# Kernel optimization log

Measured on AMD Instinct MI355X. Metric: run time of the kernel, lower is better.

The kernel has to match this reference:

```python
import jax, jax.numpy as jnp
import numpy as np

HEADS = 8
DIM_HEAD = 32  # dim // heads


def setup_inputs() -> dict:
    key = jax.random.key(0)
    ks = jax.random.split(key, 5)
    B, C, H, W = 4, 256, 48, 48
    return {
        "x": jax.random.normal(ks[0], (B, C, H, W), jnp.float32),
        "Wqkv": jax.random.normal(ks[1], (3 * C, C), jnp.float32) * (C ** -0.5),
        "bqkv": jax.random.normal(ks[2], (3 * C,), jnp.float32) * 0.02,
        "W0": jax.random.normal(ks[3], (C, C), jnp.float32) * (C ** -0.5),
        "b0": jax.random.normal(ks[4], (C,), jnp.float32) * 0.02,
    }


def reference(x, Wqkv, bqkv, W0, b0):
    b, c, h, w = x.shape
    m, d = HEADS, DIM_HEAD
    n = h * w
    scale = d ** -0.5
    # 1x1 conv == per-pixel GEMM: [b,3c,h,w]
    qkv = jnp.einsum('bchw,oc->bohw', x, Wqkv) + bqkv[None, :, None, None]
    # rearrange 'b (d k m) h w -> k b m (h w) d' (channel factors as d, then k, then m)
    qkv = qkv.reshape(b, d, 3, m, n)            # [b, d, 3, m, n]
    qkv = jnp.transpose(qkv, (2, 0, 3, 4, 1))   # [3, b, m, n, d]
    q, k, v = qkv[0], qkv[1], qkv[2]
    scores = jnp.einsum('bmid,bmjd->bmij', q, k) * scale  # [b, m, n, n]
    attn = jax.nn.softmax(scores, axis=-1)
    out = jnp.einsum('bmij,bmjd->bmid', attn, v)          # [b, m, n, d]
    # rearrange 'b m (h w) d -> b (m d) h w'
    out = jnp.transpose(out, (0, 1, 3, 2)).reshape(b, m * d, h, w)
    out = jnp.einsum('bchw,oc->bohw', out, W0) + b0[None, :, None, None]
    return out
```

## Files before the change

kernel.cpp:

```cpp
#include <hip/hip_runtime.h>
#include <hip/hip_bf16.h>

#define NPIX 2304
#define C_IN 256
#define NHEADS 8
#define DHEAD 32

typedef float f32x4 __attribute__((ext_vector_type(4)));
typedef __bf16 bf16x8 __attribute__((ext_vector_type(8)));
typedef __bf16 bf16x4 __attribute__((ext_vector_type(4)));

#if __has_builtin(__builtin_amdgcn_exp2f)
#define EXP2F(x) __builtin_amdgcn_exp2f(x)
#else
#define EXP2F(x) exp2f(x)
#endif

__device__ inline void gload_lds16(const void* g, void* l) {
    __builtin_amdgcn_global_load_lds(
        (const __attribute__((address_space(1))) unsigned int*)g,
        (__attribute__((address_space(3))) unsigned int*)l, 16, 0, 0);
}

__global__ __launch_bounds__(256) void prep_wx(
    const float* __restrict__ Wq, const float* __restrict__ W0,
    const float* __restrict__ x,
    __bf16* __restrict__ wq, __bf16* __restrict__ w0,
    __bf16* __restrict__ xt)
{
    __shared__ unsigned int lds[64 * 69];
    const int id = blockIdx.x;
    const int t  = threadIdx.x;

    if (id >= 576) {
        const int r = id - 576;
        float v;
        __bf16* dst;
        if (r < 768) { v = Wq[r * 256 + t];         dst = wq + (size_t)r * 512; }
        else         { v = W0[(r - 768) * 256 + t]; dst = w0 + (size_t)(r - 768) * 512; }
        __bf16 hb = (__bf16)v;
        dst[t]       = hb;
        dst[256 + t] = (__bf16)(v - (float)hb);
        return;
    }

    const int n0 = (id % 36) * 64;
    const int c0 = ((id / 36) & 3) * 64;
    const int b  = id / 144;
    const float* xb = x + (size_t)b * C_IN * NPIX;

    #pragma unroll
    for (int p = 0; p < 4; ++p) {
        const int r    = (t >> 4) + p * 16;
        const int ncol = (t & 15) * 4;
        float4 v = *(const float4*)&xb[(size_t)(c0 + r) * NPIX + n0 + ncol];
        float a[4] = {v.x, v.y, v.z, v.w};
        #pragma unroll
        for (int i = 0; i < 4; ++i)
            lds[r * 69 + ncol + i] =
                (unsigned int)__builtin_bit_cast(unsigned short, (__bf16)a[i]);
    }
    __syncthreads();

    #pragma unroll
    for (int p = 0; p < 2; ++p) {
        const int nn = (t >> 3) + p * 32;
        const int ch = t & 7;
        bf16x8 h8;
        #pragma unroll
        for (int i = 0; i < 8; ++i)
            h8[i] = __builtin_bit_cast(__bf16,
                        (unsigned short)lds[(ch * 8 + i) * 69 + nn]);
        *(bf16x8*)&xt[((size_t)b * NPIX + n0 + nn) * 256 + c0 + ch * 8] = h8;
    }
}

__global__ __launch_bounds__(256) void qkv_mfma(
    const __bf16* __restrict__ wq, const __bf16* __restrict__ xt,
    const float* __restrict__ bias, __bf16* __restrict__ qt,
    __bf16* __restrict__ khi, __bf16* __restrict__ vg)
{
    __shared__ alignas(16) unsigned char sm[32768];
    const int tid = threadIdx.x;
    const int l   = tid & 63;
    const int w   = tid >> 6;
    const int g   = l >> 4;
    const int c16 = l & 15;

    const int id  = blockIdx.x;
    const int xcd = id & 7;
    const int li  = id >> 3;
    const int pnl = xcd * 9 + li / 12;
    const int mtt = li % 12;
    const int b   = pnl / 18;
    const int nt  = pnl - b * 18;
    const int n0  = nt * 128;
    const int kq  = mtt >> 2;
    const int seg = (mtt & 3) * 64;

    const int wo = (w >> 1) * 32;
    const int wn = (w & 1) * 64;
    f32x4 acc[2][4] = {};

#define STG(buf, cs)                                                           \
    {                                                                          \
        unsigned char* lbs = sm + (buf) * 16384;                               \
        _Pragma("unroll")                                                      \
        for (int i = 0; i < 2; ++i) {                                          \
            const int row = i * 64 + (tid >> 2);                               \
            const int cl  = tid & 3;                                           \
            const int cg  = cl ^ (row & 3);                                    \
            const int pp  = seg + (row & 63);                                  \
            const int oA  = 24 * (pp >> 3) + 8 * kq + (pp & 7);                \
            gload_lds16(wq + (size_t)oA * 512 + i * 256 + (cs) * 32 + cg * 8,  \
                        lbs + row * 64 + cl * 16);                             \
        }                                                                      \
        _Pragma("unroll")                                                      \
        for (int i = 0; i < 2; ++i) {                                          \
            const int row = i * 64 + (tid >> 2);                               \
            const int cl  = tid & 3;                                           \
            const int cg  = cl ^ (row & 3);                                    \
            gload_lds16(xt + ((size_t)b * NPIX + n0 + row) * 256 +             \
                            (cs) * 32 + cg * 8,                                \
                        lbs + 8192 + row * 64 + cl * 16);                      \
        }                                                                      \
    }

    STG(0, 0);
    __syncthreads();
    #pragma unroll
    for (int cs = 0; cs < 8; ++cs) {
        const int buf = cs & 1;
        if (cs + 1 < 8) STG(buf ^ 1, cs + 1);
        unsigned char* lb = sm + buf * 16384;
        bf16x8 ah[2], al2[2], bf4[4];
        #pragma unroll
        for (int oi = 0; oi < 2; ++oi) {
            const int ra = wo + oi * 16 + c16;
            ah[oi]  = *(bf16x8*)(lb + ra * 64 + ((g ^ (ra & 3)) * 16));
            al2[oi] = *(bf16x8*)(lb + (64 + ra) * 64 + ((g ^ (ra & 3)) * 16));
        }
        #pragma unroll
        for (int ni = 0; ni < 4; ++ni) {
            const int rb = wn + ni * 16 + c16;
            bf4[ni] = *(bf16x8*)(lb + 8192 + rb * 64 + ((g ^ (rb & 3)) * 16));
        }
        #pragma unroll
        for (int oi = 0; oi < 2; ++oi)
            #pragma unroll
            for (int ni = 0; ni < 4; ++ni) {
                acc[oi][ni] = __builtin_amdgcn_mfma_f32_16x16x32_bf16(
                    ah[oi], bf4[ni], acc[oi][ni], 0, 0, 0);
                acc[oi][ni] = __builtin_amdgcn_mfma_f32_16x16x32_bf16(
                    al2[oi], bf4[ni], acc[oi][ni], 0, 0, 0);
            }
        __syncthreads();
    }
#undef STG

    const float qscale = 0.17677669529663687f * 1.4426950408889634f;
    #pragma unroll
    for (int oi = 0; oi < 2; ++oi) {
        #pragma unroll
        for (int rr = 0; rr < 4; ++rr) {
            const int pp = seg + wo + oi * 16 + 4 * g + rr;
            const int d  = pp >> 3;
            const int h  = pp & 7;
            const int o  = 24 * d + 8 * kq + h;
            const float bi = bias[o];
            const int bh_ = b * NHEADS + h;
            #pragma unroll
            for (int ni = 0; ni < 4; ++ni) {
                const int n = n0 + wn + ni * 16 + c16;
                const float val = acc[oi][ni][rr] + bi;
                if (kq == 0) {
                    qt[((size_t)bh_ * NPIX + n) * 32 + d] = (__bf16)(val * qscale);
                } else if (kq == 1) {
                    const int cp = ((d >> 3) + (n >> 1)) & 3;
                    khi[((size_t)bh_ * NPIX + n) * 32 + cp * 8 + (d & 7)] = (__bf16)val;
                } else {
                    const int cp = ((n >> 3) & 7) ^ (d & 7);
                    vg[((size_t)bh_ * DHEAD + d) * NPIX + (n >> 6) * 64 + cp * 8 + (n & 7)]
                        = (__bf16)val;
                }
            }
        }
    }
}

__global__ __launch_bounds__(256) void attn_mfma(
    const __bf16* __restrict__ qt, const __bf16* __restrict__ khi,
    const __bf16* __restrict__ vg,
    float* __restrict__ po, float* __restrict__ lw)
{
    __shared__ alignas(16) unsigned char sm[32768];
    const int tid = threadIdx.x;
    const int l   = tid & 63;
    const int w   = tid >> 6;
    const int g   = l >> 4;
    const int c16 = l & 15;

    const int id = blockIdx.x;
    const int lg = (id & 7) * 144 + (id >> 3);
    const int bh = lg / 36;
    const int rem = lg - bh * 36;
    const int half = rem / 18;
    const int qt_i = rem - half * 18;

    const __bf16* qb  = qt  + (size_t)bh * NPIX * 32;
    const __bf16* khb = khi + (size_t)bh * NPIX * 32;
    const __bf16* vb  = vg  + (size_t)bh * DHEAD * NPIX;

    const int q0 = qt_i * 128 + w * 32;

    bf16x8 qh[2];
    #pragma unroll
    for (int qgi = 0; qgi < 2; ++qgi)
        qh[qgi] = *(const bf16x8*)&qb[(size_t)(q0 + qgi * 16 + c16) * 32 + g * 8];

    f32x4 o[2][2] = {};
    float lsum[2] = {0.f, 0.f};

    const int vd   = w * 8 + (l >> 3);
    const int kswz = (c16 >> 1) & 3;
    unsigned char* const wsl = sm + 16384 + w * 4096;

#define STAGE(buf, kb)                                                         \
    {                                                                          \
        const int j0s = (kb) * 64;                                             \
        unsigned char* lbs = sm + (buf) * 8192;                                \
        gload_lds16(khb + (size_t)(j0s + w * 16) * 32 + l * 8, lbs + w * 1024);\
        gload_lds16(vb + (size_t)vd * NPIX + j0s + (l & 7) * 8,                \
                    lbs + 4096 + w * 1024);                                    \
    }

    const int kb0 = half * 18;
    STAGE(0, kb0);
    __syncthreads();

    for (int t = 0; t < 18; ++t) {
        const int buf = t & 1;
        if (t + 1 < 18) STAGE(buf ^ 1, kb0 + t + 1);
        unsigned char* lb = sm + buf * 8192;

        f32x4 sv[2][4];
        __builtin_amdgcn_s_setprio(1);
        #pragma unroll
        for (int f = 0; f < 4; ++f) {
            const int ko = (c16 + 16 * f) * 64 + ((g + kswz) & 3) * 16;
            bf16x8 kh8 = *(bf16x8*)(lb + ko);
            #pragma unroll
            for (int qgi = 0; qgi < 2; ++qgi) {
                f32x4 acc = {0.f, 0.f, 0.f, 0.f};
                acc = __builtin_amdgcn_mfma_f32_16x16x32_bf16(kh8, qh[qgi], acc, 0, 0, 0);
                sv[qgi][f] = acc;
            }
        }
        __builtin_amdgcn_s_setprio(0);

        #pragma unroll
        for (int qgi = 0; qgi < 2; ++qgi) {
            float rs = 0.f;
            __bf16 pb[16];
            #pragma unroll
            for (int f = 0; f < 4; ++f)
                #pragma unroll
                for (int rr = 0; rr < 4; ++rr) {
                    const float p = EXP2F(sv[qgi][f][rr]);
                    rs += p;
                    pb[f * 4 + rr] = (__bf16)p;
                }
            lsum[qgi] += rs;
            const int qrow = qgi * 16 + c16;
            #pragma unroll
            for (int f = 0; f < 4; ++f) {
                const int ch = (2 * f + (g >> 1)) ^ (c16 & 7);
                *(bf16x4*)(wsl + qrow * 128 + ch * 16 + (g & 1) * 8) =
                    *(bf16x4*)&pb[f * 4];
            }
        }

        __builtin_amdgcn_s_setprio(1);
        #pragma unroll
        for (int kc = 0; kc < 2; ++kc) {
            const int vch = (((g + 4 * kc) ^ (c16 & 7))) * 16;
            bf16x8 va0 = *(bf16x8*)(lb + 4096 + c16 * 128 + vch);
            bf16x8 va1 = *(bf16x8*)(lb + 4096 + (16 + c16) * 128 + vch);
            #pragma unroll
            for (int qgi = 0; qgi < 2; ++qgi) {
                bf16x8 pf = *(bf16x8*)(wsl + (qgi * 16 + c16) * 128 + vch);
                o[qgi][0] = __builtin_amdgcn_mfma_f32_16x16x32_bf16(va0, pf, o[qgi][0], 0, 0, 0);
                o[qgi][1] = __builtin_amdgcn_mfma_f32_16x16x32_bf16(va1, pf, o[qgi][1], 0, 0, 0);
            }
        }
        __builtin_amdgcn_s_setprio(0);

        __syncthreads();
    }
#undef STAGE

    #pragma unroll
    for (int qgi = 0; qgi < 2; ++qgi) {
        lsum[qgi] += __shfl_xor(lsum[qgi], 16);
        lsum[qgi] += __shfl_xor(lsum[qgi], 32);
        const int n = q0 + qgi * 16 + c16;
        const size_t rbase = ((size_t)(half * 32 + bh) * NPIX + n) * 32;
        #pragma unroll
        for (int dh = 0; dh < 2; ++dh)
            *(f32x4*)&po[rbase + dh * 16 + 4 * g] = o[qgi][dh];
        if (g == 0)
            lw[(size_t)(half * 32 + bh) * NPIX + n] = lsum[qgi];
    }
}

__global__ __launch_bounds__(256) void out_mfma(
    const __bf16* __restrict__ w0, const float* __restrict__ po,
    const float* __restrict__ lw, const float* __restrict__ bias,
    float* __restrict__ out)
{
    __shared__ alignas(16) unsigned char sm[34816];
    const int tid = threadIdx.x;
    const int l   = tid & 63;
    const int w   = tid >> 6;
    const int g   = l >> 4;
    const int c16 = l & 15;

    const int id  = blockIdx.x;
    const int xcd = id & 7;
    const int li  = id >> 3;
    const int pnl = xcd * 9 + (li >> 2);
    const int mt  = li & 3;
    const int b   = pnl / 18;
    const int nt  = pnl - b * 18;
    const int n0  = nt * 128;
    const int o0  = mt * 64;

    const int wo = (w >> 1) * 32;
    const int wn = (w & 1) * 64;
    f32x4 acc[2][4] = {};

    const int brow = tid >> 1;
    const int bch  = tid & 1;

#define STG_A(buf, cs)                                                         \
    {                                                                          \
        unsigned char* lbs = sm + (buf) * 17408;                               \
        _Pragma("unroll")                                                      \
        for (int i = 0; i < 2; ++i) {                                          \
            const int row = i * 64 + (tid >> 2);                               \
            const int cl  = tid & 3;                                           \
            const int cg  = cl ^ (row & 3);                                    \
            gload_lds16(w0 + (size_t)(o0 + (row & 63)) * 512 + i * 256 +       \
                            (cs) * 32 + cg * 8,                                \
                        lbs + row * 64 + cl * 16);                             \
        }                                                                      \
    }

    f32x4 r0[4], r1[4];
    float il;

#define LDB(cs)                                                                \
    {                                                                          \
        const int bh_ = b * 8 + (cs);                                          \
        const int n   = n0 + brow;                                             \
        const float l0 = lw[(size_t)bh_ * NPIX + n];                           \
        const float l1 = lw[(size_t)(32 + bh_) * NPIX + n];                    \
        il = 1.0f / (l0 + l1);                                                 \
        const float* s0 = &po[((size_t)bh_ * NPIX + n) * 32 + bch * 16];       \
        const float* s1 = &po[((size_t)(32 + bh_) * NPIX + n) * 32 + bch * 16];\
        _Pragma("unroll")                                                      \
        for (int k2 = 0; k2 < 4; ++k2) {                                       \
            r0[k2] = *(const f32x4*)(s0 + k2 * 4);                             \
            r1[k2] = *(const f32x4*)(s1 + k2 * 4);                             \
        }                                                                      \
    }

#define WRB(buf)                                                               \
    {                                                                          \
        unsigned char* lbs = sm + (buf) * 17408 + 8192;                        \
        _Pragma("unroll")                                                      \
        for (int k2 = 0; k2 < 2; ++k2) {                                       \
            bf16x8 v8;                                                         \
            _Pragma("unroll")                                                  \
            for (int e = 0; e < 4; ++e) {                                      \
                v8[e]     = (__bf16)((r0[2 * k2][e]     + r1[2 * k2][e])     * il); \
                v8[4 + e] = (__bf16)((r0[2 * k2 + 1][e] + r1[2 * k2 + 1][e]) * il); \
            }                                                                  \
            *(bf16x8*)(lbs + brow * 72 + bch * 32 + k2 * 16) = v8;             \
        }                                                                      \
    }

    STG_A(0, 0);
    LDB(0);
    WRB(0);
    __syncthreads();

    #pragma unroll
    for (int cs = 0; cs < 8; ++cs) {
        const int buf = cs & 1;
        if (cs + 1 < 8) {
            STG_A(buf ^ 1, cs + 1);
            LDB(cs + 1);
        }
        unsigned char* lb = sm + buf * 17408;
        bf16x8 ah[2], al2[2], bf4[4];
        #pragma unroll
        for (int oi = 0; oi < 2; ++oi) {
            const int ra = wo + oi * 16 + c16;
            ah[oi]  = *(bf16x8*)(lb + ra * 64 + ((g ^ (ra & 3)) * 16));
            al2[oi] = *(bf16x8*)(lb + (64 + ra) * 64 + ((g ^ (ra & 3)) * 16));
        }
        #pragma unroll
        for (int ni = 0; ni < 4; ++ni) {
            const int rb = wn + ni * 16 + c16;
            bf4[ni] = *(bf16x8*)(lb + 8192 + rb * 72 + g * 16);
        }
        #pragma unroll
        for (int oi = 0; oi < 2; ++oi)
            #pragma unroll
            for (int ni = 0; ni < 4; ++ni) {
                acc[oi][ni] = __builtin_amdgcn_mfma_f32_16x16x32_bf16(
                    ah[oi], bf4[ni], acc[oi][ni], 0, 0, 0);
                acc[oi][ni] = __builtin_amdgcn_mfma_f32_16x16x32_bf16(
                    al2[oi], bf4[ni], acc[oi][ni], 0, 0, 0);
            }
        if (cs + 1 < 8) WRB(buf ^ 1);
        __syncthreads();
    }
#undef STG_A
#undef LDB
#undef WRB

    #pragma unroll
    for (int oi = 0; oi < 2; ++oi) {
        #pragma unroll
        for (int rr = 0; rr < 4; ++rr) {
            const int o = o0 + wo + oi * 16 + 4 * g + rr;
            const float bi = bias[o];
            #pragma unroll
            for (int ni = 0; ni < 4; ++ni) {
                const int n = n0 + wn + ni * 16 + c16;
                out[((size_t)b * C_IN + o) * NPIX + n] = acc[oi][ni][rr] + bi;
            }
        }
    }
}

extern "C" void kernel_launch(void* const* d_in, const int* in_sizes, int n_in,
                              void* d_out, int out_size, void* d_ws, size_t ws_size,
                              hipStream_t stream) {
    const float* x    = (const float*)d_in[0];
    const float* Wqkv = (const float*)d_in[1];
    const float* bqkv = (const float*)d_in[2];
    const float* W0   = (const float*)d_in[3];
    const float* b0   = (const float*)d_in[4];
    float* out = (float*)d_out;

    char* ws = (char*)d_ws;
    __bf16* wq  = (__bf16*)(ws);
    __bf16* w0  = (__bf16*)(ws + 786432);
    __bf16* xt  = (__bf16*)(ws + 1048576);
    __bf16* qt  = (__bf16*)(ws + 5767168);
    __bf16* khi = (__bf16*)(ws + 10485760);
    __bf16* vg  = (__bf16*)(ws + 15204352);
    float*  po  = (float*) (ws + 19922944);
    float*  lw  = (float*) (ws + 38797312);

    prep_wx<<<dim3(1600), 256, 0, stream>>>(Wqkv, W0, x, wq, w0, xt);
    qkv_mfma<<<dim3(864), 256, 0, stream>>>(wq, xt, bqkv, qt, khi, vg);
    attn_mfma<<<dim3(1152), 256, 0, stream>>>(qt, khi, vg, po, lw);
    out_mfma<<<dim3(288), 256, 0, stream>>>(w0, po, lw, b0, out);
}
```

Measured before the change: 158.8 us.

## Drop bf16 hi/lo weight split for K/V and output projection; split attention launch

```diff
diff --git a/kernel.cpp b/kernel.cpp
--- a/kernel.cpp
+++ b/kernel.cpp
@@ -107,13 +107,16 @@
         unsigned char* lbs = sm + (buf) * 16384;                               \
         _Pragma("unroll")                                                      \
         for (int i = 0; i < 2; ++i) {                                          \
-            const int row = i * 64 + (tid >> 2);                               \
-            const int cl  = tid & 3;                                           \
-            const int cg  = cl ^ (row & 3);                                    \
-            const int pp  = seg + (row & 63);                                  \
-            const int oA  = 24 * (pp >> 3) + 8 * kq + (pp & 7);                \
-            gload_lds16(wq + (size_t)oA * 512 + i * 256 + (cs) * 32 + cg * 8,  \
-                        lbs + row * 64 + cl * 16);                             \
+            if (i == 0 || kq == 0) {                                           \
+                const int row = i * 64 + (tid >> 2);                           \
+                const int cl  = tid & 3;                                       \
+                const int cg  = cl ^ (row & 3);                                \
+                const int pp  = seg + (row & 63);                              \
+                const int oA  = 24 * (pp >> 3) + 8 * kq + (pp & 7);            \
+                gload_lds16(wq + (size_t)oA * 512 + i * 256 + (cs) * 32 +      \
+                                cg * 8,                                        \
+                            lbs + row * 64 + cl * 16);                         \
+            }                                                                  \
         }                                                                      \
         _Pragma("unroll")                                                      \
         for (int i = 0; i < 2; ++i) {                                          \
@@ -137,8 +140,9 @@
         #pragma unroll
         for (int oi = 0; oi < 2; ++oi) {
             const int ra = wo + oi * 16 + c16;
-            ah[oi]  = *(bf16x8*)(lb + ra * 64 + ((g ^ (ra & 3)) * 16));
-            al2[oi] = *(bf16x8*)(lb + (64 + ra) * 64 + ((g ^ (ra & 3)) * 16));
+            ah[oi] = *(bf16x8*)(lb + ra * 64 + ((g ^ (ra & 3)) * 16));
+            if (kq == 0)
+                al2[oi] = *(bf16x8*)(lb + (64 + ra) * 64 + ((g ^ (ra & 3)) * 16));
         }
         #pragma unroll
         for (int ni = 0; ni < 4; ++ni) {
@@ -148,12 +152,17 @@
         #pragma unroll
         for (int oi = 0; oi < 2; ++oi)
             #pragma unroll
-            for (int ni = 0; ni < 4; ++ni) {
+            for (int ni = 0; ni < 4; ++ni)
                 acc[oi][ni] = __builtin_amdgcn_mfma_f32_16x16x32_bf16(
                     ah[oi], bf4[ni], acc[oi][ni], 0, 0, 0);
-                acc[oi][ni] = __builtin_amdgcn_mfma_f32_16x16x32_bf16(
-                    al2[oi], bf4[ni], acc[oi][ni], 0, 0, 0);
-            }
+        if (kq == 0) {
+            #pragma unroll
+            for (int oi = 0; oi < 2; ++oi)
+                #pragma unroll
+                for (int ni = 0; ni < 4; ++ni)
+                    acc[oi][ni] = __builtin_amdgcn_mfma_f32_16x16x32_bf16(
+                        al2[oi], bf4[ni], acc[oi][ni], 0, 0, 0);
+        }
         __syncthreads();
     }
 #undef STG
@@ -191,7 +200,7 @@
 __global__ __launch_bounds__(256) void attn_mfma(
     const __bf16* __restrict__ qt, const __bf16* __restrict__ khi,
     const __bf16* __restrict__ vg,
-    float* __restrict__ po, float* __restrict__ lw)
+    float* __restrict__ po, float* __restrict__ lw, const int half)
 {
     __shared__ alignas(16) unsigned char sm[32768];
     const int tid = threadIdx.x;
@@ -201,11 +210,9 @@
     const int c16 = l & 15;
 
     const int id = blockIdx.x;
-    const int lg = (id & 7) * 144 + (id >> 3);
-    const int bh = lg / 36;
-    const int rem = lg - bh * 36;
-    const int half = rem / 18;
-    const int qt_i = rem - half * 18;
+    const int lg = (id & 7) * 72 + (id >> 3);
+    const int bh = lg / 18;
+    const int qt_i = lg - bh * 18;
 
     const __bf16* qb  = qt  + (size_t)bh * NPIX * 32;
     const __bf16* khb = khi + (size_t)bh * NPIX * 32;
@@ -318,7 +325,7 @@
     const float* __restrict__ lw, const float* __restrict__ bias,
     float* __restrict__ out)
 {
-    __shared__ alignas(16) unsigned char sm[34816];
+    __shared__ alignas(16) unsigned char sm[26624];
     const int tid = threadIdx.x;
     const int l   = tid & 63;
     const int w   = tid >> 6;
@@ -344,16 +351,12 @@
 
 #define STG_A(buf, cs)                                                         \
     {                                                                          \
-        unsigned char* lbs = sm + (buf) * 17408;                               \
-        _Pragma("unroll")                                                      \
-        for (int i = 0; i < 2; ++i) {                                          \
-            const int row = i * 64 + (tid >> 2);                               \
-            const int cl  = tid & 3;                                           \
-            const int cg  = cl ^ (row & 3);                                    \
-            gload_lds16(w0 + (size_t)(o0 + (row & 63)) * 512 + i * 256 +       \
-                            (cs) * 32 + cg * 8,                                \
-                        lbs + row * 64 + cl * 16);                             \
-        }                                                                      \
+        unsigned char* lbs = sm + (buf) * 13312;                               \
+        const int row = tid >> 2;                                              \
+        const int cl  = tid & 3;                                               \
+        const int cg  = cl ^ (row & 3);                                        \
+        gload_lds16(w0 + (size_t)(o0 + row) * 512 + (cs) * 32 + cg * 8,        \
+                    lbs + row * 64 + cl * 16);                                 \
     }
 
     f32x4 r0[4], r1[4];
@@ -377,7 +380,7 @@
 
 #define WRB(buf)                                                               \
     {                                                                          \
-        unsigned char* lbs = sm + (buf) * 17408 + 8192;                        \
+        unsigned char* lbs = sm + (buf) * 13312 + 4096;                        \
         _Pragma("unroll")                                                      \
         for (int k2 = 0; k2 < 2; ++k2) {                                       \
             bf16x8 v8;                                                         \
@@ -402,28 +405,24 @@
             STG_A(buf ^ 1, cs + 1);
             LDB(cs + 1);
         }
-        unsigned char* lb = sm + buf * 17408;
-        bf16x8 ah[2], al2[2], bf4[4];
+        unsigned char* lb = sm + buf * 13312;
+        bf16x8 ah[2], bf4[4];
         #pragma unroll
         for (int oi = 0; oi < 2; ++oi) {
             const int ra = wo + oi * 16 + c16;
-            ah[oi]  = *(bf16x8*)(lb + ra * 64 + ((g ^ (ra & 3)) * 16));
-            al2[oi] = *(bf16x8*)(lb + (64 + ra) * 64 + ((g ^ (ra & 3)) * 16));
+            ah[oi] = *(bf16x8*)(lb + ra * 64 + ((g ^ (ra & 3)) * 16));
         }
         #pragma unroll
         for (int ni = 0; ni < 4; ++ni) {
             const int rb = wn + ni * 16 + c16;
-            bf4[ni] = *(bf16x8*)(lb + 8192 + rb * 72 + g * 16);
+            bf4[ni] = *(bf16x8*)(lb + 4096 + rb * 72 + g * 16);
         }
         #pragma unroll
         for (int oi = 0; oi < 2; ++oi)
             #pragma unroll
-            for (int ni = 0; ni < 4; ++ni) {
+            for (int ni = 0; ni < 4; ++ni)
                 acc[oi][ni] = __builtin_amdgcn_mfma_f32_16x16x32_bf16(
                     ah[oi], bf4[ni], acc[oi][ni], 0, 0, 0);
-                acc[oi][ni] = __builtin_amdgcn_mfma_f32_16x16x32_bf16(
-                    al2[oi], bf4[ni], acc[oi][ni], 0, 0, 0);
-            }
         if (cs + 1 < 8) WRB(buf ^ 1);
         __syncthreads();
     }
@@ -468,6 +467,7 @@
 
     prep_wx<<<dim3(1600), 256, 0, stream>>>(Wqkv, W0, x, wq, w0, xt);
     qkv_mfma<<<dim3(864), 256, 0, stream>>>(wq, xt, bqkv, qt, khi, vg);
-    attn_mfma<<<dim3(1152), 256, 0, stream>>>(qt, khi, vg, po, lw);
+    attn_mfma<<<dim3(576), 256, 0, stream>>>(qt, khi, vg, po, lw, 0);
+    attn_mfma<<<dim3(576), 256, 0, stream>>>(qt, khi, vg, po, lw, 1);
     out_mfma<<<dim3(288), 256, 0, stream>>>(w0, po, lw, b0, out);
 }
```

After: 174.4 us. 9.8% more time.
